# Kernel optimization log

Measured on AMD Instinct MI355X. Metric: run time of the kernel, lower is better.

## Reference

```python
import jax, jax.numpy as jnp
import numpy as np

N_NODES = 40960
N_EDGES = 655360
IN_DIM = 128
HID = 128
HEADS = 4
CH = HID // HEADS  # per-head channels = 32
N_GRAPHS = 16
NEG_SLOPE = 0.2


def setup_inputs() -> dict:
    key = jax.random.key(0)
    ks = jax.random.split(key, 32)
    inp = {
        "x": jax.random.normal(ks[0], (N_NODES, IN_DIM), dtype=jnp.float32),
        "edge_index": jax.random.randint(ks[1], (2, N_EDGES), 0, N_NODES, dtype=jnp.int64),
        "batch_vec": jnp.sort(jax.random.randint(ks[2], (N_NODES,), 0, N_GRAPHS, dtype=jnp.int64)),
    }
    dims = [(IN_DIM, HID), (HID, HID), (HID, HID)]
    ki = 3
    for l, (din, dout) in enumerate(dims):
        s = 1.0 / np.sqrt(din)
        inp[f"Wl{l}"] = jax.random.normal(ks[ki + 0], (din, dout), dtype=jnp.float32) * s
        inp[f"bl{l}"] = jnp.zeros((dout,), dtype=jnp.float32)
        inp[f"Wr{l}"] = jax.random.normal(ks[ki + 1], (din, dout), dtype=jnp.float32) * s
        inp[f"br{l}"] = jnp.zeros((dout,), dtype=jnp.float32)
        inp[f"att{l}"] = jax.random.normal(ks[ki + 2], (HEADS, CH), dtype=jnp.float32) * (1.0 / np.sqrt(CH))
        inp[f"b{l}"] = jnp.zeros((dout,), dtype=jnp.float32)
        ki += 3
    return inp


def _gatv2_layer(x, src, dst, Wl, bl, Wr, br, att, bias):
    # GATv2Conv (PyG semantics, add_self_loops=True handled by caller's src/dst)
    n = x.shape[0]
    xl = (x @ Wl + bl).reshape(n, HEADS, CH)  # source transform
    xr = (x @ Wr + br).reshape(n, HEADS, CH)  # destination transform
    m = xl[src] + xr[dst]                      # [E, H, C]
    e = jnp.einsum("ehc,hc->eh", jax.nn.leaky_relu(m, NEG_SLOPE), att)  # [E, H]
    emax = jax.ops.segment_max(e, dst, num_segments=n)
    ex = jnp.exp(e - emax[dst])
    denom = jax.ops.segment_sum(ex, dst, num_segments=n)
    alpha = ex / denom[dst]                    # segment softmax over in-edges
    out = jax.ops.segment_sum(alpha[:, :, None] * xl[src], dst, num_segments=n)
    return out.reshape(n, HEADS * CH) + bias


def reference(x, edge_index, batch_vec,
              Wl0, bl0, Wr0, br0, att0, b0,
              Wl1, bl1, Wr1, br1, att1, b1,
              Wl2, bl2, Wr2, br2, att2, b2):
    n = x.shape[0]
    loops = jnp.arange(n, dtype=edge_index.dtype)
    src = jnp.concatenate([edge_index[0], loops])  # PyG default add_self_loops=True
    dst = jnp.concatenate([edge_index[1], loops])

    h = _gatv2_layer(x, src, dst, Wl0, bl0, Wr0, br0, att0, b0)
    h = jax.nn.relu(h)
    h = _gatv2_layer(h, src, dst, Wl1, bl1, Wr1, br1, att1, b1)
    h = jax.nn.relu(h)
    h = _gatv2_layer(h, src, dst, Wl2, bl2, Wr2, br2, att2, b2)

    # global_mean_pool over batch assignment
    sums = jax.ops.segment_sum(h, batch_vec, num_segments=N_GRAPHS)
    cnt = jax.ops.segment_sum(jnp.ones((n,), dtype=h.dtype), batch_vec, num_segments=N_GRAPHS)
    pooled = sums / jnp.maximum(cnt, 1.0)[:, None]
    return pooled, h
```

## Files before the change

### kernel.cpp

```cpp
#include <hip/hip_runtime.h>

#define NN 40960
#define NE 655360
#define ET (NE + NN)
#define D 128
#define NG 16
#define PL 16896
#define CAP 64

typedef unsigned int u32;
typedef unsigned short u16;
typedef long long i64;
typedef __attribute__((ext_vector_type(8))) short bf8v;
typedef __attribute__((ext_vector_type(4))) float f4v;

struct P18 { const void* p[18]; };

__device__ __forceinline__ float bf2f(u16 v){ return __uint_as_float(((u32)v)<<16); }
__device__ __forceinline__ u16 f2bf(float f){
  u32 u = __float_as_uint(f);
  return (u16)((u + 0x7FFFu + ((u>>16)&1u)) >> 16);
}
__device__ __forceinline__ int geti(const void* p, long long i, int f64, int bound){
  long long v = f64 ? ((const i64*)p)[i] : (long long)((const int*)p)[i];
  int x = (int)v;
  return (x < 0) ? 0 : ((x >= bound) ? bound-1 : x);
}
__device__ __forceinline__ void stf(void* p, long long i, float v, int isbf){
  if (isbf) ((u16*)p)[i] = f2bf(v); else ((float*)p)[i] = v;
}
__device__ __forceinline__ float rdf(const void* p, long long i, int isbf){
  return isbf ? bf2f(((const u16*)p)[i]) : ((const float*)p)[i];
}
__device__ __forceinline__ float4 ldb4(const u16* p){
  ushort4 u = *(const ushort4*)p;
  return make_float4(bf2f(u.x), bf2f(u.y), bf2f(u.z), bf2f(u.w));
}

__global__ void k_setup(const void* __restrict__ ei, const void* __restrict__ x,
                        int* __restrict__ flags, u32* __restrict__ cnt, float* __restrict__ pool,
                        u16* __restrict__ csr){
  int b = blockIdx.x;
  if (b == 0){
    __shared__ int nz, cn;
    if (threadIdx.x == 0){ nz = 0; cn = 0; }
    __syncthreads();
    if (((const int*)ei)[2*threadIdx.x + 1] != 0) atomicAdd(&nz, 1);
    if (threadIdx.x < 128){
      u16 v = ((const u16*)x)[2*threadIdx.x];
      int ex = (v >> 7) & 0xFF;
      if (ex >= 100 && ex <= 140) atomicAdd(&cn, 1);
    }
    __syncthreads();
    if (threadIdx.x == 0){
      flags[0] = (nz == 0) ? 1 : 0;
      flags[1] = (cn >= 64) ? 1 : 0;
    }
  } else if (b <= 2560){
    cnt[(b-1)*256 + threadIdx.x] = 0u;
  } else if (b <= 2568){
    int i = (b-2561)*256 + threadIdx.x;
    if (i < NG*D) pool[i] = 0.f;
  } else {
    if (threadIdx.x < 16) csr[(size_t)NN*CAP + threadIdx.x] = 0;
  }
}

__global__ void k_prep(P18 ps, const void* __restrict__ x, u16* __restrict__ xb,
                       float* __restrict__ prm, const void* __restrict__ ei,
                       u32* __restrict__ cnt, u16* __restrict__ csr,
                       const void* __restrict__ batch, u32* __restrict__ bnd,
                       const int* __restrict__ flags){
  int b = blockIdx.x;
  int isbf = flags[1];
  if (b == 23590){
    int g = threadIdx.x;
    if (g > NG) return;
    if (g == NG){ bnd[NG] = NN; return; }
    int f = flags[0];
    int lo = 0, hi = NN;
    while (lo < hi){
      int mid = (lo + hi) >> 1;
      if (geti(batch, mid, f, NG) < g) lo = mid + 1; else hi = mid;
    }
    bnd[g] = (u32)lo;
    return;
  }
  if (b >= 20870){
    int e = (b - 20870)*256 + threadIdx.x;
    if (e < ET){
      int f = flags[0];
      int s, dd;
      if (e < NE){ s = geti(ei, e, f, NN); dd = geti(ei, (long long)NE + e, f, NN); }
      else { s = dd = e - NE; }
      u32 pos = atomicAdd(&cnt[dd << 4], 1u);
      if (pos < CAP) csr[((size_t)dd << 6) + pos] = (u16)s;
    }
    return;
  }
  if (b >= 390){
    long long i = (long long)(b - 390)*256 + threadIdx.x;
    xb[i] = f2bf(rdf(x, i, isbf));
    return;
  }
  int l = b / 130;
  int i = (b % 130)*256 + threadIdx.x;
  const void* Wl  = ps.p[6*l+0];
  const void* bl  = ps.p[6*l+1];
  const void* Wr  = ps.p[6*l+2];
  const void* br  = ps.p[6*l+3];
  const void* att = ps.p[6*l+4];
  const void* bb  = ps.p[6*l+5];
  float* p = prm + (size_t)l*PL;
  if (i < 32768){
    int n = i >> 7, k = i & 127;
    float v = (n < 128) ? rdf(Wl, k*128 + n, isbf) : rdf(Wr, k*128 + (n - 128), isbf);
    ((u16*)p)[i] = f2bf(v);
    return;
  }
  float* fb = p + 16384;
  if (i < 33024){ int gc = i - 32768; fb[gc] = (gc < 128) ? rdf(bl, gc, isbf) : rdf(br, gc - 128, isbf); }
  else if (i < 33152) fb[256 + (i - 33024)] = rdf(att, i - 33024, isbf);
  else                fb[384 + (i - 33152)] = rdf(bb, i - 33152, isbf);
}

__global__ __launch_bounds__(256) void k_gemm(const u16* __restrict__ Xb, const float* __restrict__ pr,
                                              u16* __restrict__ xl, u16* __restrict__ xr)
{
  int wv = threadIdx.x >> 6, lane = threadIdx.x & 63;
  int row0 = blockIdx.x*64 + wv*16;
  int rA = lane & 15, ks = lane >> 4;
  const u16* wt     = (const u16*)pr;
  const float* bias = pr + 16384;

  const u16* xp = Xb + (size_t)(row0 + rA)*D + ks*8;
  bf8v a0 = *(const bf8v*)(xp);
  bf8v a1 = *(const bf8v*)(xp + 32);
  bf8v a2 = *(const bf8v*)(xp + 64);
  bf8v a3 = *(const bf8v*)(xp + 96);

  int n0 = blockIdx.y*4;
  #pragma unroll
  for (int t = 0; t < 4; ++t, ++n0){
    int gc = n0*16 + rA;
    const u16* wp = wt + (size_t)gc*D + ks*8;
    bf8v b0 = *(const bf8v*)(wp);
    bf8v b1 = *(const bf8v*)(wp + 32);
    bf8v b2 = *(const bf8v*)(wp + 64);
    bf8v b3 = *(const bf8v*)(wp + 96);
    float bv = bias[gc];
    f4v acc = {bv, bv, bv, bv};
    acc = __builtin_amdgcn_mfma_f32_16x16x32_bf16(a0, b0, acc, 0, 0, 0);
    acc = __builtin_amdgcn_mfma_f32_16x16x32_bf16(a1, b1, acc, 0, 0, 0);
    acc = __builtin_amdgcn_mfma_f32_16x16x32_bf16(a2, b2, acc, 0, 0, 0);
    acc = __builtin_amdgcn_mfma_f32_16x16x32_bf16(a3, b3, acc, 0, 0, 0);
    u16* dst = (gc < 128) ? xl : xr;
    int cc = (gc < 128) ? gc : gc - 128;
    #pragma unroll
    for (int r = 0; r < 4; ++r)
      dst[(size_t)(row0 + ks*4 + r)*D + cc] = f2bf(acc[r]);
  }
}

__global__ __launch_bounds__(256) void k_node(const u16* __restrict__ xl, const u16* __restrict__ xr,
    const u32* __restrict__ cnt, const u16* __restrict__ csr, const float* __restrict__ pr,
    u16* __restrict__ hb, float* __restrict__ hf, void* __restrict__ out,
    const int* __restrict__ flags, int last)
{
  int node = blockIdx.x*4 + (threadIdx.x >> 6);
  int lane = threadIdx.x & 63;
  int g2 = lane >> 4;
  int c = (lane & 15) * 8;
  const u16* xlc = xl + c;
  const u16* xrp = xr + (size_t)node*D + c;
  float4 xr0 = ldb4(xrp), xr1 = ldb4(xrp + 4);
  float4 at0 = *(const float4*)(pr + 16640 + c);
  float4 at1 = *(const float4*)(pr + 16640 + c + 4);
  u32 j0 = (u32)node << 6;
  u32 j1 = j0 + cnt[node << 4];

  float mx = -1e30f, ssum = 0.f;
  float4 ac0 = make_float4(0.f,0.f,0.f,0.f), ac1 = make_float4(0.f,0.f,0.f,0.f);

  u32 j = j0 + g2;
  u32 oc = ((u32)csr[j]) << 7;
  float4 g0 = ldb4(xlc + oc), g1 = ldb4(xlc + oc + 4);
  u32 on = ((u32)csr[j + 4]) << 7;

  for (; j < j1; j += 4){
    float4 n0 = ldb4(xlc + on), n1 = ldb4(xlc + on + 4);
    u32 o2 = ((u32)csr[j + 8]) << 7;

    float m, p;
    m = g0.x + xr0.x; p = fmaxf(m, 0.2f*m) * at0.x;
    m = g0.y + xr0.y; p = fmaf(fmaxf(m, 0.2f*m), at0.y, p);
    m = g0.z + xr0.z; p = fmaf(fmaxf(m, 0.2f*m), at0.z, p);
    m = g0.w + xr0.w; p = fmaf(fmaxf(m, 0.2f*m), at0.w, p);
    m = g1.x + xr1.x; p = fmaf(fmaxf(m, 0.2f*m), at1.x, p);
    m = g1.y + xr1.y; p = fmaf(fmaxf(m, 0.2f*m), at1.y, p);
    m = g1.z + xr1.z; p = fmaf(fmaxf(m, 0.2f*m), at1.z, p);
    m = g1.w + xr1.w; p = fmaf(fmaxf(m, 0.2f*m), at1.w, p);
    p += __shfl_xor(p, 1, 64);
    p += __shfl_xor(p, 2, 64);
    if (p > mx + 8.f){
      float eo = __expf(mx - p);
      ssum *= eo;
      ac0.x *= eo; ac0.y *= eo; ac0.z *= eo; ac0.w *= eo;
      ac1.x *= eo; ac1.y *= eo; ac1.z *= eo; ac1.w *= eo;
      mx = p;
    }
    float en = __expf(p - mx);
    ssum += en;
    ac0.x = fmaf(en, g0.x, ac0.x); ac0.y = fmaf(en, g0.y, ac0.y);
    ac0.z = fmaf(en, g0.z, ac0.z); ac0.w = fmaf(en, g0.w, ac0.w);
    ac1.x = fmaf(en, g1.x, ac1.x); ac1.y = fmaf(en, g1.y, ac1.y);
    ac1.z = fmaf(en, g1.z, ac1.z); ac1.w = fmaf(en, g1.w, ac1.w);
    g0 = n0; g1 = n1; on = o2;
  }

  #pragma unroll
  for (int off = 16; off < 64; off <<= 1){
    float mo  = __shfl_xor(mx, off, 64);
    float so  = __shfl_xor(ssum, off, 64);
    float b0x = __shfl_xor(ac0.x, off, 64), b0y = __shfl_xor(ac0.y, off, 64);
    float b0z = __shfl_xor(ac0.z, off, 64), b0w = __shfl_xor(ac0.w, off, 64);
    float b1x = __shfl_xor(ac1.x, off, 64), b1y = __shfl_xor(ac1.y, off, 64);
    float b1z = __shfl_xor(ac1.z, off, 64), b1w = __shfl_xor(ac1.w, off, 64);
    float nm = fmaxf(mx, mo);
    float e0 = __expf(mx - nm), e1 = __expf(mo - nm);
    ssum  = ssum*e0 + so*e1;
    ac0.x = ac0.x*e0 + b0x*e1; ac0.y = ac0.y*e0 + b0y*e1;
    ac0.z = ac0.z*e0 + b0z*e1; ac0.w = ac0.w*e0 + b0w*e1;
    ac1.x = ac1.x*e0 + b1x*e1; ac1.y = ac1.y*e0 + b1y*e1;
    ac1.z = ac1.z*e0 + b1z*e1; ac1.w = ac1.w*e0 + b1w*e1;
    mx = nm;
  }

  if (lane < 16){
    float inv = 1.0f / fmaxf(ssum, 1e-30f);
    float4 bv0 = *(const float4*)(pr + 16768 + c);
    float4 bv1 = *(const float4*)(pr + 16768 + c + 4);
    float4 v0 = make_float4(ac0.x*inv + bv0.x, ac0.y*inv + bv0.y,
                            ac0.z*inv + bv0.z, ac0.w*inv + bv0.w);
    float4 v1 = make_float4(ac1.x*inv + bv1.x, ac1.y*inv + bv1.y,
                            ac1.z*inv + bv1.z, ac1.w*inv + bv1.w);
    if (!last){
      v0.x = fmaxf(v0.x, 0.f); v0.y = fmaxf(v0.y, 0.f);
      v0.z = fmaxf(v0.z, 0.f); v0.w = fmaxf(v0.w, 0.f);
      v1.x = fmaxf(v1.x, 0.f); v1.y = fmaxf(v1.y, 0.f);
      v1.z = fmaxf(v1.z, 0.f); v1.w = fmaxf(v1.w, 0.f);
      u16* hp = hb + (size_t)node*D + c;
      *(ushort4*)(hp)     = make_ushort4(f2bf(v0.x), f2bf(v0.y), f2bf(v0.z), f2bf(v0.w));
      *(ushort4*)(hp + 4) = make_ushort4(f2bf(v1.x), f2bf(v1.y), f2bf(v1.z), f2bf(v1.w));
    } else {
      float* fp = hf + (size_t)node*D + c;
      *(float4*)(fp)     = v0;
      *(float4*)(fp + 4) = v1;
      int isbf = flags[1];
      long long o = (long long)NG*D + (long long)node*D + c;
      stf(out, o+0, v0.x, isbf); stf(out, o+1, v0.y, isbf);
      stf(out, o+2, v0.z, isbf); stf(out, o+3, v0.w, isbf);
      stf(out, o+4, v1.x, isbf); stf(out, o+5, v1.y, isbf);
      stf(out, o+6, v1.z, isbf); stf(out, o+7, v1.w, isbf);
    }
  }
}

__global__ __launch_bounds__(256) void k_pool1(const float* __restrict__ h, const u32* __restrict__ bnd,
                                               float* __restrict__ pool){
  __shared__ float red[256];
  int g = blockIdx.x >> 4, sl = blockIdx.x & 15;
  int ch = threadIdx.x & 127, ro = threadIdx.x >> 7;
  u32 b0 = bnd[g], b1 = bnd[g + 1];
  float acc = 0.f;
  for (u32 r = b0 + sl*2 + ro; r < b1; r += 32) acc += h[(size_t)r*D + ch];
  red[threadIdx.x] = acc;
  __syncthreads();
  if (threadIdx.x < 128)
    unsafeAtomicAdd(&pool[g*D + ch], red[threadIdx.x] + red[threadIdx.x + 128]);
}

__global__ void k_pool2(const float* __restrict__ pool, const u32* __restrict__ bnd,
                        void* __restrict__ out, const int* __restrict__ flags){
  int i = blockIdx.x*256 + threadIdx.x;
  if (i >= NG*D) return;
  int g = i >> 7;
  float c = (float)(bnd[g + 1] - bnd[g]);
  stf(out, i, pool[i] / fmaxf(c, 1.f), flags[1]);
}

extern "C" void kernel_launch(void* const* d_in, const int* in_sizes, int n_in,
                              void* d_out, int out_size, void* d_ws, size_t ws_size,
                              hipStream_t stream) {
  const void* x     = d_in[0];
  const void* ei    = d_in[1];
  const void* batch = d_in[2];

  const long long nf = (long long)NN*D + 3*PL + NG*D;
  const long long nh = (long long)NN*D*3;
  const long long nu = (long long)NN*16 + (NG + 1) + 2;
  const long long nc = (long long)NN*CAP + 16;
  if (ws_size < (size_t)nf*4 + (size_t)nh*2 + (size_t)nu*4 + (size_t)nc*2 + 256) return;

  float* ws    = (float*)d_ws;
  float* xf    = ws;
  u16*  xb    = (u16*)(xf + (size_t)NN*D);
  u16*  xl    = xb + (size_t)NN*D;
  u16*  xr    = xl + (size_t)NN*D;
  float* prm   = (float*)(xr + (size_t)NN*D);
  float* pool  = prm + 3*PL;
  u32*  cnt    = (u32*)(pool + NG*D);
  u32*  bnd    = cnt + (size_t)NN*16;
  int*  flags  = (int*)(bnd + (NG + 1));
  u16*  csr    = (u16*)(flags + 2);

  k_setup<<<2570, 256, 0, stream>>>(ei, x, flags, cnt, pool, csr);
  P18 ps;
  for (int i = 0; i < 18; ++i) ps.p[i] = d_in[3 + i];
  k_prep<<<23591, 256, 0, stream>>>(ps, x, xb, prm, ei, cnt, csr, batch, bnd, flags);

  for (int l = 0; l < 3; ++l){
    k_gemm<<<dim3(NN/64, 4), 256, 0, stream>>>(xb, prm + (size_t)l*PL, xl, xr);
    k_node<<<NN/4, 256, 0, stream>>>(xl, xr, cnt, csr, prm + (size_t)l*PL,
                                     xb, xf, d_out, flags, l == 2);
  }
  k_pool1<<<NG*16, 256, 0, stream>>>(xf, bnd, pool);
  k_pool2<<<8, 256, 0, stream>>>(pool, bnd, d_out, flags);
}
```

Before: 282.1 us.

## Fuse input bf16 conversion into first GEMM and partition CSR build by destination

Drops the separate pass that converted x to bf16 inside k_prep; the first-layer GEMM now reads fp32 x directly and converts fragments in registers. The edge-scatter CSR build now runs 8 passes over all edges, each pass only inserting edges whose destination falls in one of 8 node ranges, to localise atomics and CSR writes. This costs reading the edge list 8 times and makes every pass re-read indices, in exchange for better cache locality of the atomic counters and scattered writes.

Result: faster. 259.1 us (median of 2 runs) (-8.2%).

```diff
diff --git a/kernel.cpp b/kernel.cpp
--- a/kernel.cpp
+++ b/kernel.cpp
@@ -7,6 +7,8 @@
 #define NG 16
 #define PL 16896
 #define CAP 64
+#define SCB 2720
+#define PSZ 5120
 
 typedef unsigned int u32;
 typedef unsigned short u16;
@@ -35,6 +37,17 @@
 __device__ __forceinline__ float4 ldb4(const u16* p){
   ushort4 u = *(const ushort4*)p;
   return make_float4(bf2f(u.x), bf2f(u.y), bf2f(u.z), bf2f(u.w));
+}
+__device__ __forceinline__ bf8v ldfrag(const void* X, size_t off, int isf32){
+  if (!isf32) return *(const bf8v*)((const u16*)X + off);
+  const float* fp = (const float*)X + off;
+  float4 u = *(const float4*)fp, v = *(const float4*)(fp + 4);
+  bf8v r;
+  r[0] = (short)f2bf(u.x); r[1] = (short)f2bf(u.y);
+  r[2] = (short)f2bf(u.z); r[3] = (short)f2bf(u.w);
+  r[4] = (short)f2bf(v.x); r[5] = (short)f2bf(v.y);
+  r[6] = (short)f2bf(v.z); r[7] = (short)f2bf(v.w);
+  return r;
 }
 
 __global__ void k_setup(const void* __restrict__ ei, const void* __restrict__ x,
@@ -66,14 +79,27 @@
   }
 }
 
-__global__ void k_prep(P18 ps, const void* __restrict__ x, u16* __restrict__ xb,
-                       float* __restrict__ prm, const void* __restrict__ ei,
+__global__ void k_prep(P18 ps, float* __restrict__ prm, const void* __restrict__ ei,
                        u32* __restrict__ cnt, u16* __restrict__ csr,
                        const void* __restrict__ batch, u32* __restrict__ bnd,
                        const int* __restrict__ flags){
   int b = blockIdx.x;
   int isbf = flags[1];
-  if (b == 23590){
+  if (b >= 391){
+    int pb = b - 391;
+    u32 plo = (u32)(pb & 7) * PSZ;
+    int e = (pb >> 3)*256 + threadIdx.x;
+    int f = flags[0];
+    int s, dd;
+    if (e < NE){ s = geti(ei, e, f, NN); dd = geti(ei, (long long)NE + e, f, NN); }
+    else { s = dd = e - NE; }
+    if ((u32)dd - plo < PSZ){
+      u32 pos = atomicAdd(&cnt[dd << 4], 1u);
+      if (pos < CAP) csr[((size_t)dd << 6) + pos] = (u16)s;
+    }
+    return;
+  }
+  if (b == 390){
     int g = threadIdx.x;
     if (g > NG) return;
     if (g == NG){ bnd[NG] = NN; return; }
@@ -84,23 +110,6 @@
       if (geti(batch, mid, f, NG) < g) lo = mid + 1; else hi = mid;
     }
     bnd[g] = (u32)lo;
-    return;
-  }
-  if (b >= 20870){
-    int e = (b - 20870)*256 + threadIdx.x;
-    if (e < ET){
-      int f = flags[0];
-      int s, dd;
-      if (e < NE){ s = geti(ei, e, f, NN); dd = geti(ei, (long long)NE + e, f, NN); }
-      else { s = dd = e - NE; }
-      u32 pos = atomicAdd(&cnt[dd << 4], 1u);
-      if (pos < CAP) csr[((size_t)dd << 6) + pos] = (u16)s;
-    }
-    return;
-  }
-  if (b >= 390){
-    long long i = (long long)(b - 390)*256 + threadIdx.x;
-    xb[i] = f2bf(rdf(x, i, isbf));
     return;
   }
   int l = b / 130;
@@ -124,20 +133,22 @@
   else                fb[384 + (i - 33152)] = rdf(bb, i - 33152, isbf);
 }
 
-__global__ __launch_bounds__(256) void k_gemm(const u16* __restrict__ Xb, const float* __restrict__ pr,
-                                              u16* __restrict__ xl, u16* __restrict__ xr)
+__global__ __launch_bounds__(256) void k_gemm(const void* __restrict__ Xv, const float* __restrict__ pr,
+                                              u16* __restrict__ xl, u16* __restrict__ xr,
+                                              const int* __restrict__ flags, int lay0)
 {
   int wv = threadIdx.x >> 6, lane = threadIdx.x & 63;
   int row0 = blockIdx.x*64 + wv*16;
   int rA = lane & 15, ks = lane >> 4;
+  int isf32 = lay0 ? (flags[1] == 0) : 0;
   const u16* wt     = (const u16*)pr;
   const float* bias = pr + 16384;
 
-  const u16* xp = Xb + (size_t)(row0 + rA)*D + ks*8;
-  bf8v a0 = *(const bf8v*)(xp);
-  bf8v a1 = *(const bf8v*)(xp + 32);
-  bf8v a2 = *(const bf8v*)(xp + 64);
-  bf8v a3 = *(const bf8v*)(xp + 96);
+  size_t xoff = (size_t)(row0 + rA)*D + ks*8;
+  bf8v a0 = ldfrag(Xv, xoff,      isf32);
+  bf8v a1 = ldfrag(Xv, xoff + 32, isf32);
+  bf8v a2 = ldfrag(Xv, xoff + 64, isf32);
+  bf8v a3 = ldfrag(Xv, xoff + 96, isf32);
 
   int n0 = blockIdx.y*4;
   #pragma unroll
@@ -317,10 +328,11 @@
   k_setup<<<2570, 256, 0, stream>>>(ei, x, flags, cnt, pool, csr);
   P18 ps;
   for (int i = 0; i < 18; ++i) ps.p[i] = d_in[3 + i];
-  k_prep<<<23591, 256, 0, stream>>>(ps, x, xb, prm, ei, cnt, csr, batch, bnd, flags);
+  k_prep<<<391 + 8*SCB, 256, 0, stream>>>(ps, prm, ei, cnt, csr, batch, bnd, flags);
 
   for (int l = 0; l < 3; ++l){
-    k_gemm<<<dim3(NN/64, 4), 256, 0, stream>>>(xb, prm + (size_t)l*PL, xl, xr);
+    const void* Xin = (l == 0) ? x : (const void*)xb;
+    k_gemm<<<dim3(NN/64, 4), 256, 0, stream>>>(Xin, prm + (size_t)l*PL, xl, xr, flags, l == 0);
     k_node<<<NN/4, 256, 0, stream>>>(xl, xr, cnt, csr, prm + (size_t)l*PL,
                                      xb, xf, d_out, flags, l == 2);
   }
```
